# Kernel optimization log

Measured on AMD Instinct MI355X. Metric: run time of the kernel, lower is better.

The kernel has to match this reference:

```python
import jax, jax.numpy as jnp
import numpy as np
from functools import partial

K = 20
NEG_SLOPE = 0.2
BN_EPS = 1e-5


def knn_idx(x, k):
    # x: (B, C, N). Negative squared distance, top-k neighbors (self included).
    inner = jnp.einsum('bcn,bcm->bnm', x, x)            # (B,N,N)
    xx = jnp.sum(x * x, axis=1)                          # (B,N)
    neg_dist = 2.0 * inner - xx[:, :, None] - xx[:, None, :]
    _, idx = jax.lax.top_k(neg_dist, k)                  # (B,N,k)
    return idx


def get_graph_feature(x, k):
    # x: (B, C, N) -> edge features (B, N, k, 2C) = [x_j - x_i, x_i]
    B = x.shape[0]
    idx = knn_idx(x, k)                                  # (B,N,k)
    xt = jnp.transpose(x, (0, 2, 1))                     # (B,N,C)
    nbr = xt[jnp.arange(B)[:, None, None], idx]          # (B,N,k,C)
    xi = jnp.broadcast_to(xt[:, :, None, :], nbr.shape)
    return jnp.concatenate([nbr - xi, xi], axis=-1)


def edge_block(x, W, g, b, k):
    # 1x1 conv + BatchNorm2d (training stats) + LeakyReLU + max over k.
    e = get_graph_feature(x, k)                          # (B,N,k,2C)
    y = jnp.einsum('bnkc,oc->bonk', e, W)                # (B,Cout,N,k)
    mean = jnp.mean(y, axis=(0, 2, 3), keepdims=True)
    var = jnp.mean((y - mean) ** 2, axis=(0, 2, 3), keepdims=True)
    y = (y - mean) * jax.lax.rsqrt(var + BN_EPS)
    y = y * g[None, :, None, None] + b[None, :, None, None]
    y = jnp.where(y > 0, y, NEG_SLOPE * y)
    return jnp.max(y, axis=-1)                           # (B,Cout,N)


def setup_inputs() -> dict:
    key = jax.random.key(0)
    ks = jax.random.split(key, 4)
    B, C, N = 4, 3, 4096
    ch = [64, 64, 128]
    x = jax.random.normal(ks[0], (B, C, N), dtype=jnp.float32)
    W0 = jax.random.normal(ks[1], (ch[0], 2 * C), dtype=jnp.float32) * 0.1
    W1 = jax.random.normal(ks[2], (ch[1], 2 * ch[0]), dtype=jnp.float32) * 0.1
    W2 = jax.random.normal(ks[3], (ch[2], 2 * ch[1]), dtype=jnp.float32) * 0.1
    return {
        'x': x,
        'W0': W0, 'g0': jnp.ones(ch[0]), 'b0': jnp.zeros(ch[0]),
        'W1': W1, 'g1': jnp.ones(ch[1]), 'b1': jnp.zeros(ch[1]),
        'W2': W2, 'g2': jnp.ones(ch[2]), 'b2': jnp.zeros(ch[2]),
    }


def reference(x, W0, g0, b0, W1, g1, b1, W2, g2, b2):
    feats = []
    cur = x
    for (W, g, b) in ((W0, g0, b0), (W1, g1, b1), (W2, g2, b2)):
        cur = edge_block(cur, W, g, b, K)
        feats.append(cur)
    return jnp.concatenate(feats, axis=1)                # (B, 256, N)
```

## Files before the change

### kernel.cpp

```cpp
#include <hip/hip_runtime.h>
#include <math.h>

#define NN 4096
#define BB 4
#define KK 20
#define OUTC 256
#define GN (BB*NN)

template<int C>
__global__ void __launch_bounds__(256) xx_kernel(const float* __restrict__ x, int bstride,
                                                 float* __restrict__ xxo) {
  int i = blockIdx.x*256 + threadIdx.x;
  int b = i >> 12, n = i & (NN-1);
  const float* xp = x + (size_t)b*bstride + n;
  float s = 0.f;
#pragma unroll
  for (int c = 0; c < C; ++c) { float v = xp[(size_t)c*NN]; s = fmaf(v, v, s); }
  xxo[i] = s;
}

__device__ __forceinline__ unsigned ord_u32(float v) {
  unsigned b = __float_as_uint(v);
  return (b & 0x80000000u) ? ~b : (b | 0x80000000u);
}

template<int S>
__device__ __forceinline__ bool extract_top20(const float (&sv)[S], const int (&si)[S],
                                              float od, int* __restrict__ outp,
                                              unsigned long long lmask) {
  unsigned u[S];
#pragma unroll
  for (int k = 0; k < S; ++k) u[k] = ord_u32(sv[k]);
  unsigned T = 0u;
#pragma unroll 1
  for (int bit = 31; bit >= 0; --bit) {
    unsigned Tp = T | (1u << bit);
    int c = 0;
#pragma unroll
    for (int k = 0; k < S; ++k) c += __popcll(__ballot(u[k] >= Tp));
    if (c >= KK) T = Tp;
  }
  int cgt = 0;
#pragma unroll
  for (int k = 0; k < S; ++k) cgt += __popcll(__ballot(u[k] > T));
  const int r = KK - cgt;
  int A = 0;
#pragma unroll 1
  for (int bit = 11; bit >= 0; --bit) {
    int Ap = A | (1 << bit);
    int c = 0;
#pragma unroll
    for (int k = 0; k < S; ++k) c += __popcll(__ballot(u[k] == T && si[k] < Ap));
    if (c < r) A = Ap;
  }
  int base = 0;
#pragma unroll
  for (int k = 0; k < S; ++k) {
    bool kp = (u[k] > T) || (u[k] == T && si[k] <= A);
    unsigned long long mk = __ballot(kp);
    int pos = base + __popcll(mk & lmask);
    if (kp) outp[pos] = si[k];
    base += __popcll(mk);
  }
  return __ballot(ord_u32(od) >= T) != 0ull;
}

template<int C>
__global__ void __launch_bounds__(256)
__attribute__((amdgpu_waves_per_eu(2, 2)))
knn6_kernel(const float* __restrict__ x, int bstride,
            const float* __restrict__ xxb,
            int* __restrict__ idx_out,
            int* __restrict__ flag_cnt,
            int* __restrict__ flag_list) {
  constexpr int CC = (C < 16) ? C : 16;
  constexpr int S = 4;
  __shared__ float cand[CC][512];
  __shared__ float xm_lds[512];
  __shared__ float xq_lds[32];
  const int tid = threadIdx.x;
  const int wq = tid >> 6, lane = tid & 63;
  const unsigned long long lmask = (1ull << lane) - 1ull;
  const int qb = blockIdx.x;
  const int b = qb >> 7, n0 = (qb & 127) << 5;
  const float* xb  = x + (size_t)b*bstride;
  const float* xxr = xxb + b*NN;
  const int uwq = __builtin_amdgcn_readfirstlane(wq);
  const float* qp = xb + n0 + uwq*8;

  if (tid < 32) xq_lds[tid] = xxr[n0 + tid];
  __syncthreads();
  float xq[8];
#pragma unroll
  for (int i = 0; i < 8; ++i) xq[i] = xq_lds[wq*8 + i];

  float sv[8][S]; int si[8][S]; float od[8];
#pragma unroll
  for (int i = 0; i < 8; ++i) {
    od[i] = -INFINITY;
#pragma unroll
    for (int k = 0; k < S; ++k) { sv[i][k] = -INFINITY; si[i][k] = 0x7fffffff; }
  }

  for (int t = 0; t < NN/512; ++t) {
    const int mt0 = t*512;
    float acc[8][8];
#pragma unroll
    for (int i = 0; i < 8; ++i)
#pragma unroll
      for (int j = 0; j < 8; ++j) acc[i][j] = 0.f;

    for (int cc0 = 0; cc0 < C; cc0 += CC) {
      __syncthreads();
      for (int v = tid; v < CC*128; v += 256) {
        int c = v >> 7, mc = (v & 127) * 4;
        *reinterpret_cast<float4*>(&cand[c][mc]) =
          *reinterpret_cast<const float4*>(&xb[(size_t)(cc0 + c)*NN + mt0 + mc]);
      }
      if (cc0 == 0 && tid < 128)
        *reinterpret_cast<float4*>(&xm_lds[tid*4]) =
          *reinterpret_cast<const float4*>(&xxr[mt0 + tid*4]);
      __syncthreads();
#pragma unroll 8
      for (int c = 0; c < CC; ++c) {
        const float* qcp = qp + (size_t)(cc0 + c)*NN;
        float qq[8];
#pragma unroll
        for (int i = 0; i < 8; ++i) qq[i] = qcp[i];
        float4 ca = *reinterpret_cast<const float4*>(&cand[c][lane*4]);
        float4 cb = *reinterpret_cast<const float4*>(&cand[c][256 + lane*4]);
        float mm[8] = {ca.x, ca.y, ca.z, ca.w, cb.x, cb.y, cb.z, cb.w};
#pragma unroll
        for (int i = 0; i < 8; ++i)
#pragma unroll
          for (int j = 0; j < 8; ++j) acc[i][j] = fmaf(qq[i], mm[j], acc[i][j]);
      }
    }

    float4 xma = *reinterpret_cast<const float4*>(&xm_lds[lane*4]);
    float4 xmb = *reinterpret_cast<const float4*>(&xm_lds[256 + lane*4]);
    float xmv[8] = {xma.x, xma.y, xma.z, xma.w, xmb.x, xmb.y, xmb.z, xmb.w};

#pragma unroll
    for (int i = 0; i < 8; ++i) {
#pragma unroll
      for (int j = 0; j < 8; ++j) {
        const float d = 2.f*acc[i][j] - xq[i] - xmv[j];
        const int mi = mt0 + ((j < 4) ? (lane*4 + j) : (256 + lane*4 + (j - 4)));
        od[i] = fmaxf(od[i], fminf(d, sv[i][3]));
        bool c0 = d > sv[i][0], c1 = d > sv[i][1], c2 = d > sv[i][2], c3 = d > sv[i][3];
        sv[i][3] = c2 ? sv[i][2] : (c3 ? d : sv[i][3]);  si[i][3] = c2 ? si[i][2] : (c3 ? mi : si[i][3]);
        sv[i][2] = c1 ? sv[i][1] : (c2 ? d : sv[i][2]);  si[i][2] = c1 ? si[i][1] : (c2 ? mi : si[i][2]);
        sv[i][1] = c0 ? sv[i][0] : (c1 ? d : sv[i][1]);  si[i][1] = c0 ? si[i][0] : (c1 ? mi : si[i][1]);
        sv[i][0] = c0 ? d : sv[i][0];                    si[i][0] = c0 ? mi : si[i][0];
      }
    }
  }

#pragma unroll
  for (int i = 0; i < 8; ++i) {
    const int q = n0 + wq*8 + i;
    int* outp = idx_out + (size_t)(b*NN + q)*KK;
    bool need_fix = extract_top20<S>(sv[i], si[i], od[i], outp, lmask);
    if (need_fix) {
      if (lane == 0) { int p = atomicAdd(flag_cnt, 1); flag_list[p & 4095] = b*NN + q; }
    }
  }
}

template<int C>
__global__ void __launch_bounds__(256) knn_fix_kernel(const float* __restrict__ x, int bstride,
                                                      const float* __restrict__ xxb,
                                                      const int* __restrict__ flag_cnt,
                                                      const int* __restrict__ flag_list,
                                                      int* __restrict__ idx_out) {
  __shared__ float redv[4]; __shared__ int redi[4];
  const int tid = threadIdx.x;
  const int wid = tid >> 6, lane = tid & 63;
  const int cnt = flag_cnt[0] < 4096 ? flag_cnt[0] : 4096;
  for (int f = blockIdx.x; f < cnt; f += gridDim.x) {
    const int qn = flag_list[f];
    const int b = qn >> 12, n = qn & (NN-1);
    const float* xb  = x + (size_t)b*bstride;
    const float* xxr = xxb + b*NN;
    float acc[16];
#pragma unroll
    for (int jj = 0; jj < 16; ++jj) acc[jj] = 0.f;
    for (int c = 0; c < C; ++c) {
      const float qc = xb[(size_t)c*NN + n];
      const float* row = xb + (size_t)c*NN + tid;
#pragma unroll
      for (int jj = 0; jj < 16; ++jj) acc[jj] = fmaf(qc, row[256*jj], acc[jj]);
    }
    const float xq = xxr[n];
    float dv[16]; int di[16]; unsigned used = 0;
#pragma unroll
    for (int jj = 0; jj < 16; ++jj) {
      dv[jj] = 2.f*acc[jj] - xq - xxr[tid + 256*jj];
      di[jj] = tid + 256*jj;
    }
    for (int r = 0; r < KK; ++r) {
      float bv = -INFINITY; int bi = 0x7fffffff;
#pragma unroll
      for (int jj = 0; jj < 16; ++jj) {
        bool ok = !((used >> jj) & 1);
        bool bet = ok && (dv[jj] > bv || (dv[jj] == bv && di[jj] < bi));
        bv = bet ? dv[jj] : bv; bi = bet ? di[jj] : bi;
      }
#pragma unroll
      for (int s = 1; s < 64; s <<= 1) {
        float ov = __shfl_xor(bv, s, 64);
        int   oi = __shfl_xor(bi, s, 64);
        if (ov > bv || (ov == bv && oi < bi)) { bv = ov; bi = oi; }
      }
      if (lane == 0) { redv[wid] = bv; redi[wid] = bi; }
      __syncthreads();
#pragma unroll
      for (int w = 0; w < 4; ++w) {
        float ov = redv[w]; int oi = redi[w];
        if (ov > bv || (ov == bv && oi < bi)) { bv = ov; bi = oi; }
      }
      __syncthreads();
      if ((bi & 255) == tid) used |= 1u << (bi >> 8);
      if (tid == 0) idx_out[(size_t)qn*KK + r] = bi;
    }
  }
}

template<int C, int O>
__global__ void __launch_bounds__(256) pq_kernel(const float* __restrict__ x, int bstride,
                                                 const float* __restrict__ W,
                                                 float* __restrict__ P, float* __restrict__ Q) {
  constexpr int CC = (C < 32) ? C : 32;
  constexpr int NPP = 256 / O;
  constexpr int NITER = 64 / NPP;
  __shared__ float xt[C*64];
  __shared__ float w1t[CC*O];
  __shared__ float wdt[CC*O];
  const int tid = threadIdx.x;
  const int g0 = blockIdx.x*64;
  const int b = g0 >> 12, n0 = g0 & (NN-1);
  for (int i = tid; i < C*64; i += 256) {
    int c = i >> 6, j = i & 63;
    xt[i] = x[(size_t)b*bstride + (size_t)c*NN + (n0 + j)];
  }
  const int o = tid % O;
  const int ns = tid / O;
  float ap[NITER], aq[NITER];
#pragma unroll
  for (int i = 0; i < NITER; ++i) { ap[i] = 0.f; aq[i] = 0.f; }
  for (int cc = 0; cc < C; cc += CC) {
    __syncthreads();
    for (int i = tid; i < CC*O; i += 256) {
      int oo = i % O, c = i / O;
      float w1 = W[oo*(2*C) + cc + c];
      float w2 = W[oo*(2*C) + C + cc + c];
      w1t[c*O + oo] = w1;
      wdt[c*O + oo] = w2 - w1;
    }
    __syncthreads();
#pragma unroll
    for (int np = 0; np < NITER; ++np) {
      const int nl = np*NPP + ns;
#pragma unroll
      for (int c = 0; c < CC; ++c) {
        float xv = xt[(cc + c)*64 + nl];
        ap[np] = fmaf(xv, w1t[c*O + o], ap[np]);
        aq[np] = fmaf(xv, wdt[c*O + o], aq[np]);
      }
    }
  }
#pragma unroll
  for (int np = 0; np < NITER; ++np) {
    const int nl = np*NPP + ns;
    size_t row = (size_t)(g0 + nl)*O + o;
    P[row] = ap[np];
    Q[row] = aq[np];
  }
}

template<int O>
__global__ void __launch_bounds__(256) stats_kernel(const float* __restrict__ P,
                                                    const float* __restrict__ Q,
                                                    const int* __restrict__ idxb,
                                                    float* __restrict__ ymax,
                                                    float* __restrict__ ymin,
                                                    float* __restrict__ parts) {
  constexpr int NPB = 256 / O;
  __shared__ float ls[256], ls2[256];
  const int tid = threadIdx.x;
  const int o = tid % O, ns = tid / O;
  const int g = blockIdx.x*NPB + ns;
  const int b = g >> 12;
  const float qvv = Q[(size_t)g*O + o];
  const int* ip = idxb + (size_t)g*KK;
  const float* Pb = P + (size_t)b*NN*O;
  float s = 0.f, s2 = 0.f, mx = -INFINITY, mn = INFINITY;
#pragma unroll 4
  for (int k = 0; k < KK; ++k) {
    int m = ip[k];
    float yv = Pb[(size_t)m*O + o] + qvv;
    s += yv; s2 = fmaf(yv, yv, s2);
    mx = fmaxf(mx, yv); mn = fminf(mn, yv);
  }
  ymax[(size_t)g*O + o] = mx;
  ymin[(size_t)g*O + o] = mn;
  ls[tid] = s; ls2[tid] = s2;
  __syncthreads();
  if (ns == 0) {
#pragma unroll
    for (int j = 1; j < NPB; ++j) { s += ls[j*O + o]; s2 += ls2[j*O + o]; }
    parts[(size_t)blockIdx.x*2*O + o] = s;
    parts[(size_t)blockIdx.x*2*O + O + o] = s2;
  }
}

template<int O>
__global__ void __launch_bounds__(256) reduce_kernel(const float* __restrict__ parts, int nblocks,
                                                     const float* __restrict__ gg,
                                                     const float* __restrict__ bbp,
                                                     float* __restrict__ chan) {
  __shared__ double sh[512];
  const int o = blockIdx.x, t = threadIdx.x;
  double S = 0.0, S2 = 0.0;
  for (int i = t; i < nblocks; i += 256) {
    S  += (double)parts[(size_t)i*2*O + o];
    S2 += (double)parts[(size_t)i*2*O + O + o];
  }
  sh[t] = S; sh[256+t] = S2;
  __syncthreads();
  for (int s = 128; s > 0; s >>= 1) {
    if (t < s) { sh[t] += sh[t+s]; sh[256+t] += sh[256+t+s]; }
    __syncthreads();
  }
  if (t == 0) {
    const double M = (double)BB*NN*KK;
    double mean = sh[0]/M;
    double var  = sh[256]/M - mean*mean;
    double inv  = 1.0/sqrt(var + 1e-5);
    double A  = (double)gg[o]*inv;
    double Bc = (double)bbp[o] - mean*A;
    chan[2*o]   = (float)A;
    chan[2*o+1] = (float)Bc;
  }
}

template<int O>
__global__ void __launch_bounds__(256) final_kernel(const float* __restrict__ ymax,
                                                    const float* __restrict__ ymin,
                                                    const float* __restrict__ chan,
                                                    float* __restrict__ out, int cbase) {
  __shared__ float buf[64*(O+1)];
  const int tid = threadIdx.x;
  const int g0 = blockIdx.x*64;
  const int b = g0 >> 12, n0 = g0 & (NN-1);
  for (int i = tid; i < 64*O; i += 256) {
    int o = i % O, nl = i / O;
    size_t r = (size_t)(g0 + nl)*O + o;
    float A = chan[2*o], Bc = chan[2*o+1];
    float v = (A > 0.f) ? ymax[r] : ymin[r];
    float y = fmaf(A, v, Bc);
    buf[nl*(O+1) + o] = (y > 0.f) ? y : 0.2f*y;
  }
  __syncthreads();
  for (int i = tid; i < 64*O; i += 256) {
    int nl = i & 63, o = i >> 6;
    out[(size_t)b*(OUTC*NN) + (size_t)(cbase + o)*NN + (n0 + nl)] = buf[nl*(O+1) + o];
  }
}

extern "C" void kernel_launch(void* const* d_in, const int* in_sizes, int n_in,
                              void* d_out, int out_size, void* d_ws, size_t ws_size,
                              hipStream_t stream) {
  (void)in_sizes; (void)n_in; (void)out_size; (void)ws_size;
  const float* x  = (const float*)d_in[0];
  const float* W0 = (const float*)d_in[1];
  const float* g0 = (const float*)d_in[2];
  const float* b0 = (const float*)d_in[3];
  const float* W1 = (const float*)d_in[4];
  const float* g1 = (const float*)d_in[5];
  const float* b1 = (const float*)d_in[6];
  const float* W2 = (const float*)d_in[7];
  const float* g2 = (const float*)d_in[8];
  const float* b2 = (const float*)d_in[9];
  float* out = (float*)d_out;
  char* ws = (char*)d_ws;

  float* xxb  = (float*)(ws);
  int*   idxb = (int*)  (ws + ((size_t)1<<20));
  float* P    = (float*)(ws + ((size_t)4<<20));
  float* Q    = (float*)(ws + ((size_t)12<<20));
  float* ymax = (float*)(ws + ((size_t)20<<20));
  float* ymin = (float*)(ws + ((size_t)28<<20));
  float* prts = (float*)(ws + ((size_t)36<<20));
  float* chan = (float*)(ws + ((size_t)44<<20));
  int*   fcnt = (int*)  (ws + ((size_t)45<<20));
  int*   flst = (int*)  (ws + ((size_t)45<<20) + 64);

  hipMemsetAsync(fcnt, 0, 3*sizeof(int), stream);

  xx_kernel<3><<<GN/256, 256, 0, stream>>>(x, 3*NN, xxb);
  knn6_kernel<3><<<GN/32, 256, 0, stream>>>(x, 3*NN, xxb, idxb, fcnt+0, flst+0*4096);
  knn_fix_kernel<3><<<64, 256, 0, stream>>>(x, 3*NN, xxb, fcnt+0, flst+0*4096, idxb);
  pq_kernel<3,64><<<GN/64, 256, 0, stream>>>(x, 3*NN, W0, P, Q);
  stats_kernel<64><<<GN/4, 256, 0, stream>>>(P, Q, idxb, ymax, ymin, prts);
  reduce_kernel<64><<<64, 256, 0, stream>>>(prts, GN/4, g0, b0, chan);
  final_kernel<64><<<GN/64, 256, 0, stream>>>(ymax, ymin, chan, out, 0);

  const float* x1 = out;
  xx_kernel<64><<<GN/256, 256, 0, stream>>>(x1, OUTC*NN, xxb);
  knn6_kernel<64><<<GN/32, 256, 0, stream>>>(x1, OUTC*NN, xxb, idxb, fcnt+1, flst+1*4096);
  knn_fix_kernel<64><<<64, 256, 0, stream>>>(x1, OUTC*NN, xxb, fcnt+1, flst+1*4096, idxb);
  pq_kernel<64,64><<<GN/64, 256, 0, stream>>>(x1, OUTC*NN, W1, P, Q);
  stats_kernel<64><<<GN/4, 256, 0, stream>>>(P, Q, idxb, ymax, ymin, prts);
  reduce_kernel<64><<<64, 256, 0, stream>>>(prts, GN/4, g1, b1, chan);
  final_kernel<64><<<GN/64, 256, 0, stream>>>(ymax, ymin, chan, out, 64);

  const float* x2 = out + (size_t)64*NN;
  xx_kernel<64><<<GN/256, 256, 0, stream>>>(x2, OUTC*NN, xxb);
  knn6_kernel<64><<<GN/32, 256, 0, stream>>>(x2, OUTC*NN, xxb, idxb, fcnt+2, flst+2*4096);
  knn_fix_kernel<64><<<64, 256, 0, stream>>>(x2, OUTC*NN, xxb, fcnt+2, flst+2*4096, idxb);
  pq_kernel<64,128><<<GN/64, 256, 0, stream>>>(x2, OUTC*NN, W2, P, Q);
  stats_kernel<128><<<GN/2, 256, 0, stream>>>(P, Q, idxb, ymax, ymin, prts);
  reduce_kernel<128><<<128, 256, 0, stream>>>(prts, GN/2, g2, b2, chan);
  final_kernel<128><<<GN/64, 256, 0, stream>>>(ymax, ymin, chan, out, 128);
}
```

Measured before the change: 927.9 us.

## Split KNN candidate range across two blocks and merge partial top-k lists

Each query block now scans only half of the candidate points, so twice as many blocks run. Each half writes its own partial top-20 values and indices to a workspace, and a new merge kernel picks the final top-20 from the 40 candidates per query. Occupancy is also raised from 2 to 3 waves per EU. The aim is better GPU fill and less serial work per block, at the cost of an extra kernel launch, extra global traffic, and register pressure from the higher occupancy target. The fix-up flag now fires when either half overflows its per-lane list, and the fix kernel then overwrites the merged result.

```diff
diff --git a/kernel.cpp b/kernel.cpp
--- a/kernel.cpp
+++ b/kernel.cpp
@@ -25,9 +25,10 @@
 }
 
 template<int S>
-__device__ __forceinline__ bool extract_top20(const float (&sv)[S], const int (&si)[S],
-                                              float od, int* __restrict__ outp,
-                                              unsigned long long lmask) {
+__device__ __forceinline__ bool extract_topk(const float (&sv)[S], const int (&si)[S],
+                                             float od, float* __restrict__ voutp,
+                                             int* __restrict__ ioutp,
+                                             unsigned long long lmask) {
   unsigned u[S];
 #pragma unroll
   for (int k = 0; k < S; ++k) u[k] = ord_u32(sv[k]);
@@ -59,7 +60,7 @@
     bool kp = (u[k] > T) || (u[k] == T && si[k] <= A);
     unsigned long long mk = __ballot(kp);
     int pos = base + __popcll(mk & lmask);
-    if (kp) outp[pos] = si[k];
+    if (kp) { voutp[pos] = sv[k]; ioutp[pos] = si[k]; }
     base += __popcll(mk);
   }
   return __ballot(ord_u32(od) >= T) != 0ull;
@@ -67,12 +68,11 @@
 
 template<int C>
 __global__ void __launch_bounds__(256)
-__attribute__((amdgpu_waves_per_eu(2, 2)))
-knn6_kernel(const float* __restrict__ x, int bstride,
+__attribute__((amdgpu_waves_per_eu(3, 3)))
+knn7_kernel(const float* __restrict__ x, int bstride,
             const float* __restrict__ xxb,
-            int* __restrict__ idx_out,
-            int* __restrict__ flag_cnt,
-            int* __restrict__ flag_list) {
+            float* __restrict__ hval, int* __restrict__ hidx,
+            int* __restrict__ flag_cnt, int* __restrict__ flag_list) {
   constexpr int CC = (C < 16) ? C : 16;
   constexpr int S = 4;
   __shared__ float cand[CC][512];
@@ -81,7 +81,8 @@
   const int tid = threadIdx.x;
   const int wq = tid >> 6, lane = tid & 63;
   const unsigned long long lmask = (1ull << lane) - 1ull;
-  const int qb = blockIdx.x;
+  const int qb = blockIdx.x >> 1;
+  const int h  = blockIdx.x & 1;
   const int b = qb >> 7, n0 = (qb & 127) << 5;
   const float* xb  = x + (size_t)b*bstride;
   const float* xxr = xxb + b*NN;
@@ -102,8 +103,8 @@
     for (int k = 0; k < S; ++k) { sv[i][k] = -INFINITY; si[i][k] = 0x7fffffff; }
   }
 
-  for (int t = 0; t < NN/512; ++t) {
-    const int mt0 = t*512;
+  for (int t = 0; t < 4; ++t) {
+    const int mt0 = h*(NN/2) + t*512;
     float acc[8][8];
 #pragma unroll
     for (int i = 0; i < 8; ++i)
@@ -160,12 +161,42 @@
 #pragma unroll
   for (int i = 0; i < 8; ++i) {
     const int q = n0 + wq*8 + i;
-    int* outp = idx_out + (size_t)(b*NN + q)*KK;
-    bool need_fix = extract_top20<S>(sv[i], si[i], od[i], outp, lmask);
+    const size_t rowo = ((size_t)(b*NN + q)*2 + h)*KK;
+    bool need_fix = extract_topk<S>(sv[i], si[i], od[i], hval + rowo, hidx + rowo, lmask);
     if (need_fix) {
       if (lane == 0) { int p = atomicAdd(flag_cnt, 1); flag_list[p & 4095] = b*NN + q; }
     }
   }
+}
+
+__global__ void __launch_bounds__(256) knn_merge_kernel(const float* __restrict__ hval,
+                                                        const int* __restrict__ hidx,
+                                                        int* __restrict__ idx_out) {
+  const int tid = threadIdx.x;
+  const int w = tid >> 6, l = tid & 63;
+  const unsigned long long lmask = (1ull << l) - 1ull;
+  const int qn = blockIdx.x*4 + w;
+  float v = -INFINITY; int id = 0x7fffffff;
+  if (l < 2*KK) { v = hval[(size_t)qn*2*KK + l]; id = hidx[(size_t)qn*2*KK + l]; }
+  unsigned u = ord_u32(v);
+  unsigned T = 0u;
+#pragma unroll 1
+  for (int bit = 31; bit >= 0; --bit) {
+    unsigned Tp = T | (1u << bit);
+    if (__popcll(__ballot(u >= Tp)) >= KK) T = Tp;
+  }
+  int cgt = __popcll(__ballot(u > T));
+  const int r = KK - cgt;
+  int A = 0;
+#pragma unroll 1
+  for (int bit = 11; bit >= 0; --bit) {
+    int Ap = A | (1 << bit);
+    if (__popcll(__ballot(u == T && id < Ap)) < r) A = Ap;
+  }
+  bool kp = (u > T) || (u == T && id <= A);
+  unsigned long long mk = __ballot(kp);
+  int pos = __popcll(mk & lmask);
+  if (kp) idx_out[(size_t)qn*KK + pos] = id;
 }
 
 template<int C>
@@ -393,6 +424,8 @@
   float* ymax = (float*)(ws + ((size_t)20<<20));
   float* ymin = (float*)(ws + ((size_t)28<<20));
   float* prts = (float*)(ws + ((size_t)36<<20));
+  float* hval = (float*)(ws + ((size_t)36<<20));
+  int*   hidx = (int*)  (ws + ((size_t)40<<20));
   float* chan = (float*)(ws + ((size_t)44<<20));
   int*   fcnt = (int*)  (ws + ((size_t)45<<20));
   int*   flst = (int*)  (ws + ((size_t)45<<20) + 64);
@@ -400,7 +433,8 @@
   hipMemsetAsync(fcnt, 0, 3*sizeof(int), stream);
 
   xx_kernel<3><<<GN/256, 256, 0, stream>>>(x, 3*NN, xxb);
-  knn6_kernel<3><<<GN/32, 256, 0, stream>>>(x, 3*NN, xxb, idxb, fcnt+0, flst+0*4096);
+  knn7_kernel<3><<<GN/16, 256, 0, stream>>>(x, 3*NN, xxb, hval, hidx, fcnt+0, flst+0*4096);
+  knn_merge_kernel<<<GN/4, 256, 0, stream>>>(hval, hidx, idxb);
   knn_fix_kernel<3><<<64, 256, 0, stream>>>(x, 3*NN, xxb, fcnt+0, flst+0*4096, idxb);
   pq_kernel<3,64><<<GN/64, 256, 0, stream>>>(x, 3*NN, W0, P, Q);
   stats_kernel<64><<<GN/4, 256, 0, stream>>>(P, Q, idxb, ymax, ymin, prts);
@@ -409,7 +443,8 @@
 
   const float* x1 = out;
   xx_kernel<64><<<GN/256, 256, 0, stream>>>(x1, OUTC*NN, xxb);
-  knn6_kernel<64><<<GN/32, 256, 0, stream>>>(x1, OUTC*NN, xxb, idxb, fcnt+1, flst+1*4096);
+  knn7_kernel<64><<<GN/16, 256, 0, stream>>>(x1, OUTC*NN, xxb, hval, hidx, fcnt+1, flst+1*4096);
+  knn_merge_kernel<<<GN/4, 256, 0, stream>>>(hval, hidx, idxb);
   knn_fix_kernel<64><<<64, 256, 0, stream>>>(x1, OUTC*NN, xxb, fcnt+1, flst+1*4096, idxb);
   pq_kernel<64,64><<<GN/64, 256, 0, stream>>>(x1, OUTC*NN, W1, P, Q);
   stats_kernel<64><<<GN/4, 256, 0, stream>>>(P, Q, idxb, ymax, ymin, prts);
@@ -418,7 +453,8 @@
 
   const float* x2 = out + (size_t)64*NN;
   xx_kernel<64><<<GN/256, 256, 0, stream>>>(x2, OUTC*NN, xxb);
-  knn6_kernel<64><<<GN/32, 256, 0, stream>>>(x2, OUTC*NN, xxb, idxb, fcnt+2, flst+2*4096);
+  knn7_kernel<64><<<GN/16, 256, 0, stream>>>(x2, OUTC*NN, xxb, hval, hidx, fcnt+2, flst+2*4096);
+  knn_merge_kernel<<<GN/4, 256, 0, stream>>>(hval, hidx, idxb);
   knn_fix_kernel<64><<<64, 256, 0, stream>>>(x2, OUTC*NN, xxb, fcnt+2, flst+2*4096, idxb);
   pq_kernel<64,128><<<GN/64, 256, 0, stream>>>(x2, OUTC*NN, W2, P, Q);
   stats_kernel<128><<<GN/2, 256, 0, stream>>>(P, Q, idxb, ymax, ymin, prts);
```

Measured after the change: 1.005 ms. 1.08x slower.

## Double-buffer KNN candidate tiles with register prefetch across flattened tile/channel loop

Applied to the files above, without the earlier changes.

Restructures the KNN distance kernel's main loop into one flattened loop over (point tile, channel chunk) stages. The next stage's candidate data is prefetched from global memory into registers while the current chunk is computed, then written into the other half of a double-buffered LDS array. The channel chunk shrinks from 16 to 8 so the extra registers and LDS fit. The candidate squared norms are now read straight from global memory instead of being staged in LDS. This is meant to hide global-load latency behind the FMA work, at the cost of more register pressure and one more barrier per stage.

```diff
diff --git a/kernel.cpp b/kernel.cpp
--- a/kernel.cpp
+++ b/kernel.cpp
@@ -68,15 +68,18 @@
 template<int C>
 __global__ void __launch_bounds__(256)
 __attribute__((amdgpu_waves_per_eu(2, 2)))
-knn6_kernel(const float* __restrict__ x, int bstride,
+knn8_kernel(const float* __restrict__ x, int bstride,
             const float* __restrict__ xxb,
             int* __restrict__ idx_out,
             int* __restrict__ flag_cnt,
             int* __restrict__ flag_list) {
-  constexpr int CC = (C < 16) ? C : 16;
+  constexpr int CC = (C < 8) ? C : 8;
+  constexpr int NCH = C / CC;
+  constexpr int NT = NN/512;
+  constexpr int P = NT * NCH;
+  constexpr int NL = (CC*128 + 255)/256;
   constexpr int S = 4;
-  __shared__ float cand[CC][512];
-  __shared__ float xm_lds[512];
+  __shared__ float cand[2][CC][512];
   __shared__ float xq_lds[32];
   const int tid = threadIdx.x;
   const int wq = tid >> 6, lane = tid & 63;
@@ -102,59 +105,104 @@
     for (int k = 0; k < S; ++k) { sv[i][k] = -INFINITY; si[i][k] = 0x7fffffff; }
   }
 
-  for (int t = 0; t < NN/512; ++t) {
-    const int mt0 = t*512;
-    float acc[8][8];
-#pragma unroll
-    for (int i = 0; i < 8; ++i)
-#pragma unroll
-      for (int j = 0; j < 8; ++j) acc[i][j] = 0.f;
-
-    for (int cc0 = 0; cc0 < C; cc0 += CC) {
-      __syncthreads();
-      for (int v = tid; v < CC*128; v += 256) {
-        int c = v >> 7, mc = (v & 127) * 4;
-        *reinterpret_cast<float4*>(&cand[c][mc]) =
-          *reinterpret_cast<const float4*>(&xb[(size_t)(cc0 + c)*NN + mt0 + mc]);
-      }
-      if (cc0 == 0 && tid < 128)
-        *reinterpret_cast<float4*>(&xm_lds[tid*4]) =
-          *reinterpret_cast<const float4*>(&xxr[mt0 + tid*4]);
-      __syncthreads();
-#pragma unroll 8
-      for (int c = 0; c < CC; ++c) {
-        const float* qcp = qp + (size_t)(cc0 + c)*NN;
-        float qq[8];
-#pragma unroll
-        for (int i = 0; i < 8; ++i) qq[i] = qcp[i];
-        float4 ca = *reinterpret_cast<const float4*>(&cand[c][lane*4]);
-        float4 cb = *reinterpret_cast<const float4*>(&cand[c][256 + lane*4]);
-        float mm[8] = {ca.x, ca.y, ca.z, ca.w, cb.x, cb.y, cb.z, cb.w};
-#pragma unroll
-        for (int i = 0; i < 8; ++i)
-#pragma unroll
-          for (int j = 0; j < 8; ++j) acc[i][j] = fmaf(qq[i], mm[j], acc[i][j]);
-      }
-    }
-
-    float4 xma = *reinterpret_cast<const float4*>(&xm_lds[lane*4]);
-    float4 xmb = *reinterpret_cast<const float4*>(&xm_lds[256 + lane*4]);
-    float xmv[8] = {xma.x, xma.y, xma.z, xma.w, xmb.x, xmb.y, xmb.z, xmb.w};
-
-#pragma unroll
-    for (int i = 0; i < 8; ++i) {
-#pragma unroll
-      for (int j = 0; j < 8; ++j) {
-        const float d = 2.f*acc[i][j] - xq[i] - xmv[j];
-        const int mi = mt0 + ((j < 4) ? (lane*4 + j) : (256 + lane*4 + (j - 4)));
-        od[i] = fmaxf(od[i], fminf(d, sv[i][3]));
-        bool c0 = d > sv[i][0], c1 = d > sv[i][1], c2 = d > sv[i][2], c3 = d > sv[i][3];
-        sv[i][3] = c2 ? sv[i][2] : (c3 ? d : sv[i][3]);  si[i][3] = c2 ? si[i][2] : (c3 ? mi : si[i][3]);
-        sv[i][2] = c1 ? sv[i][1] : (c2 ? d : sv[i][2]);  si[i][2] = c1 ? si[i][1] : (c2 ? mi : si[i][2]);
-        sv[i][1] = c0 ? sv[i][0] : (c1 ? d : sv[i][1]);  si[i][1] = c0 ? si[i][0] : (c1 ? mi : si[i][1]);
-        sv[i][0] = c0 ? d : sv[i][0];                    si[i][0] = c0 ? mi : si[i][0];
-      }
-    }
+  float acc[8][8];
+
+  {
+    float4 r0[NL];
+#pragma unroll
+    for (int l = 0; l < NL; ++l) {
+      int idx = tid + l*256;
+      if (idx < CC*128) {
+        int c = idx >> 7, mc = (idx & 127)*4;
+        r0[l] = *reinterpret_cast<const float4*>(&xb[(size_t)c*NN + mc]);
+      }
+    }
+#pragma unroll
+    for (int l = 0; l < NL; ++l) {
+      int idx = tid + l*256;
+      if (idx < CC*128) {
+        int c = idx >> 7, mc = (idx & 127)*4;
+        *reinterpret_cast<float4*>(&cand[0][c][mc]) = r0[l];
+      }
+    }
+  }
+  __syncthreads();
+
+#pragma unroll 1
+  for (int p = 0; p < P; ++p) {
+    const int tp = p / NCH, cp = p - tp*NCH;
+    const int buf = p & 1;
+    const int mt0 = tp*512;
+    const int cbase = cp*CC;
+
+    float4 rB[NL];
+    const int pn = p + 1;
+    if (pn < P) {
+      const int tpn = pn / NCH, cpn = pn - tpn*NCH;
+      const int mt0n = tpn*512, cbn = cpn*CC;
+#pragma unroll
+      for (int l = 0; l < NL; ++l) {
+        int idx = tid + l*256;
+        if (idx < CC*128) {
+          int c = idx >> 7, mc = (idx & 127)*4;
+          rB[l] = *reinterpret_cast<const float4*>(&xb[(size_t)(cbn + c)*NN + mt0n + mc]);
+        }
+      }
+    }
+
+    if (cp == 0) {
+#pragma unroll
+      for (int i = 0; i < 8; ++i)
+#pragma unroll
+        for (int j = 0; j < 8; ++j) acc[i][j] = 0.f;
+    }
+#pragma unroll
+    for (int c = 0; c < CC; ++c) {
+      const float* qcp = qp + (size_t)(cbase + c)*NN;
+      float qq[8];
+#pragma unroll
+      for (int i = 0; i < 8; ++i) qq[i] = qcp[i];
+      float4 ca = *reinterpret_cast<const float4*>(&cand[buf][c][lane*4]);
+      float4 cb = *reinterpret_cast<const float4*>(&cand[buf][c][256 + lane*4]);
+      float mm[8] = {ca.x, ca.y, ca.z, ca.w, cb.x, cb.y, cb.z, cb.w};
+#pragma unroll
+      for (int i = 0; i < 8; ++i)
+#pragma unroll
+        for (int j = 0; j < 8; ++j) acc[i][j] = fmaf(qq[i], mm[j], acc[i][j]);
+    }
+
+    if (cp == NCH - 1) {
+      float4 xma = *reinterpret_cast<const float4*>(&xxr[mt0 + lane*4]);
+      float4 xmb = *reinterpret_cast<const float4*>(&xxr[mt0 + 256 + lane*4]);
+      float xmv[8] = {xma.x, xma.y, xma.z, xma.w, xmb.x, xmb.y, xmb.z, xmb.w};
+#pragma unroll
+      for (int i = 0; i < 8; ++i) {
+#pragma unroll
+        for (int j = 0; j < 8; ++j) {
+          const float d = 2.f*acc[i][j] - xq[i] - xmv[j];
+          const int mi = mt0 + ((j < 4) ? (lane*4 + j) : (256 + lane*4 + (j - 4)));
+          od[i] = fmaxf(od[i], fminf(d, sv[i][3]));
+          bool c0 = d > sv[i][0], c1 = d > sv[i][1], c2 = d > sv[i][2], c3 = d > sv[i][3];
+          sv[i][3] = c2 ? sv[i][2] : (c3 ? d : sv[i][3]);  si[i][3] = c2 ? si[i][2] : (c3 ? mi : si[i][3]);
+          sv[i][2] = c1 ? sv[i][1] : (c2 ? d : sv[i][2]);  si[i][2] = c1 ? si[i][1] : (c2 ? mi : si[i][2]);
+          sv[i][1] = c0 ? sv[i][0] : (c1 ? d : sv[i][1]);  si[i][1] = c0 ? si[i][0] : (c1 ? mi : si[i][1]);
+          sv[i][0] = c0 ? d : sv[i][0];                    si[i][0] = c0 ? mi : si[i][0];
+        }
+      }
+    }
+
+    __syncthreads();
+    if (pn < P) {
+#pragma unroll
+      for (int l = 0; l < NL; ++l) {
+        int idx = tid + l*256;
+        if (idx < CC*128) {
+          int c = idx >> 7, mc = (idx & 127)*4;
+          *reinterpret_cast<float4*>(&cand[buf ^ 1][c][mc]) = rB[l];
+        }
+      }
+    }
+    __syncthreads();
   }
 
 #pragma unroll
@@ -400,7 +448,7 @@
   hipMemsetAsync(fcnt, 0, 3*sizeof(int), stream);
 
   xx_kernel<3><<<GN/256, 256, 0, stream>>>(x, 3*NN, xxb);
-  knn6_kernel<3><<<GN/32, 256, 0, stream>>>(x, 3*NN, xxb, idxb, fcnt+0, flst+0*4096);
+  knn8_kernel<3><<<GN/32, 256, 0, stream>>>(x, 3*NN, xxb, idxb, fcnt+0, flst+0*4096);
   knn_fix_kernel<3><<<64, 256, 0, stream>>>(x, 3*NN, xxb, fcnt+0, flst+0*4096, idxb);
   pq_kernel<3,64><<<GN/64, 256, 0, stream>>>(x, 3*NN, W0, P, Q);
   stats_kernel<64><<<GN/4, 256, 0, stream>>>(P, Q, idxb, ymax, ymin, prts);
@@ -409,7 +457,7 @@
 
   const float* x1 = out;
   xx_kernel<64><<<GN/256, 256, 0, stream>>>(x1, OUTC*NN, xxb);
-  knn6_kernel<64><<<GN/32, 256, 0, stream>>>(x1, OUTC*NN, xxb, idxb, fcnt+1, flst+1*4096);
+  knn8_kernel<64><<<GN/32, 256, 0, stream>>>(x1, OUTC*NN, xxb, idxb, fcnt+1, flst+1*4096);
   knn_fix_kernel<64><<<64, 256, 0, stream>>>(x1, OUTC*NN, xxb, fcnt+1, flst+1*4096, idxb);
   pq_kernel<64,64><<<GN/64, 256, 0, stream>>>(x1, OUTC*NN, W1, P, Q);
   stats_kernel<64><<<GN/4, 256, 0, stream>>>(P, Q, idxb, ymax, ymin, prts);
@@ -418,7 +466,7 @@
 
   const float* x2 = out + (size_t)64*NN;
   xx_kernel<64><<<GN/256, 256, 0, stream>>>(x2, OUTC*NN, xxb);
-  knn6_kernel<64><<<GN/32, 256, 0, stream>>>(x2, OUTC*NN, xxb, idxb, fcnt+2, flst+2*4096);
+  knn8_kernel<64><<<GN/32, 256, 0, stream>>>(x2, OUTC*NN, xxb, idxb, fcnt+2, flst+2*4096);
   knn_fix_kernel<64><<<64, 256, 0, stream>>>(x2, OUTC*NN, xxb, fcnt+2, flst+2*4096, idxb);
   pq_kernel<64,128><<<GN/64, 256, 0, stream>>>(x2, OUTC*NN, W2, P, Q);
   stats_kernel<128><<<GN/2, 256, 0, stream>>>(P, Q, idxb, ymax, ymin, prts);
```

Measured after the change: 1.093 ms. 1.18x slower.
